# Kernel optimization log

Measured on AMD Instinct MI355X. Metric: run time of the kernel, lower is better.

The kernel has to match this reference:

```python
import jax, jax.numpy as jnp
from jax import lax
import numpy as np

IOU_THRESHOLD = 0.35
SCORE_THRESHOLD = 0.5


def _pairwise_iou(b):
    # b: [N,4] boxes in (ymin, xmin, ymax, xmax) convention (tf boxes)
    y1, x1, y2, x2 = b[:, 0], b[:, 1], b[:, 2], b[:, 3]
    area = (y2 - y1) * (x2 - x1)
    iy1 = jnp.maximum(y1[:, None], y1[None, :])
    ix1 = jnp.maximum(x1[:, None], x1[None, :])
    iy2 = jnp.minimum(y2[:, None], y2[None, :])
    ix2 = jnp.minimum(x2[:, None], x2[None, :])
    inter = jnp.maximum(iy2 - iy1, 0.0) * jnp.maximum(ix2 - ix1, 0.0)
    union = area[:, None] + area[None, :] - inter
    return jnp.where(union > 0, inter / union, 0.0)  # [N,N]


def _nms_sample_image(scores, boxes, anchors_wh, num_samples):
    # scores [N], boxes [N,4], anchors_wh [N,2]
    N = scores.shape[0]
    order = jnp.argsort(-scores)  # descending by score, like tf NMS
    s = scores[order]
    b = boxes[order]
    a = anchors_wh[order]
    valid = s > SCORE_THRESHOLD
    iou = _pairwise_iou(b)  # [N,N] on score-sorted boxes
    idx = jnp.arange(N)

    # greedy suppression: box i kept iff valid and no earlier kept box overlaps > thr
    def step(keep, i):
        suppressed = jnp.any(keep & (idx < i) & (iou[i] > IOU_THRESHOLD))
        return keep.at[i].set(valid[i] & ~suppressed), None

    keep, _ = lax.scan(step, jnp.zeros(N, dtype=bool), idx)

    # gather kept entries in (descending-score) order, then pad/slice to num_samples
    rank = jnp.cumsum(keep) - 1  # output slot for each kept entry
    slot = jnp.where(keep, jnp.minimum(rank, num_samples), num_samples)
    vals = jnp.concatenate([s[:, None], b, a], axis=1)  # [N,7]
    out = jnp.zeros((num_samples + 1, 7), vals.dtype).at[slot].set(vals)
    return out[:num_samples]  # [num_samples, 7] = (score | box(4) | anchor_wh(2))


def reference(scores, boxes, anchors, num_samples):
    # scores [B,H,W,1], boxes [B,H,W,4], anchors [B,H,W,4] (last 2 chans = w,h)
    B = scores.shape[0]
    sc = scores.reshape(B, -1)
    bx = boxes.reshape(B, -1, 4)
    an = anchors[..., 2:].reshape(B, -1, 2)
    out = jax.vmap(lambda s, b, a: _nms_sample_image(s, b, a, num_samples))(sc, bx, an)
    return out  # [B, num_samples, 7]


def setup_inputs() -> dict:
    key = jax.random.key(0)
    k1, k2, k3, k4, k5 = jax.random.split(key, 5)
    B, H, W = 8, 64, 64
    scores = jax.random.uniform(k1, (B, H, W, 1), dtype=jnp.float32)
    # well-formed tf boxes: ymin<ymax, xmin<xmax in [0,1]
    ymin = jax.random.uniform(k2, (B, H, W, 1), dtype=jnp.float32) * 0.8
    xmin = jax.random.uniform(k3, (B, H, W, 1), dtype=jnp.float32) * 0.8
    hh = jax.random.uniform(k4, (B, H, W, 1), dtype=jnp.float32) * 0.18 + 0.02
    ww = jax.random.uniform(k5, (B, H, W, 1), dtype=jnp.float32) * 0.18 + 0.02
    boxes = jnp.concatenate([ymin, xmin, ymin + hh, xmin + ww], axis=-1)
    # anchors: [cy, cx, w, h]-style; only last two channels are used
    k6 = jax.random.fold_in(key, 6)
    anchors = jax.random.uniform(k6, (B, H, W, 4), dtype=jnp.float32) * 0.25 + 0.05
    return {"scores": scores, "boxes": boxes, "anchors": anchors, "num_samples": 300}
```

## Files before the change

### kernel.cpp

```cpp
#include <hip/hip_runtime.h>

static constexpr float kIouT = 0.35f;
static constexpr float kScoreT = 0.5f;
static constexpr int kMaxNW = 48;
static constexpr int kStride = 49;
static constexpr int kMaxKeep = 512;

__device__ __forceinline__ float iou_f(const float4 a, const float4 b) {
  float areaA = __fmul_rn(a.z - a.x, a.w - a.y);
  float areaB = __fmul_rn(b.z - b.x, b.w - b.y);
  float iy1 = fmaxf(a.x, b.x);
  float ix1 = fmaxf(a.y, b.y);
  float iy2 = fminf(a.z, b.z);
  float ix2 = fminf(a.w, b.w);
  float dy = fmaxf(iy2 - iy1, 0.0f);
  float dx = fmaxf(ix2 - ix1, 0.0f);
  float inter = __fmul_rn(dy, dx);
  float uni = (areaA + areaB) - inter;
  return (uni > 0.0f) ? __fdiv_rn(inter, uni) : 0.0f;
}

__global__ __launch_bounds__(256)
void nms_count_kernel(const float* __restrict__ scores, int* __restrict__ Mcnt,
                      int N) {
  __shared__ int part[4];
  const int img = blockIdx.x, tid = threadIdx.x, lane = tid & 63, wv = tid >> 6;
  const float4* sc4 = (const float4*)(scores + (size_t)img * N);
  int c = 0;
  for (int q = tid; q < (N >> 2); q += 256) {
    float4 v = sc4[q];
    c += (v.x > kScoreT) + (v.y > kScoreT) + (v.z > kScoreT) + (v.w > kScoreT);
  }
#pragma unroll
  for (int off = 1; off < 64; off <<= 1) c += __shfl_xor(c, off, 64);
  if (lane == 0) part[wv] = c;
  __syncthreads();
  if (tid == 0) Mcnt[img] = part[0] + part[1] + part[2] + part[3];
}

__global__ __launch_bounds__(256)
void nms_rank_kernel(const float* __restrict__ scores,
                     const float4* __restrict__ boxes,
                     unsigned long long* __restrict__ skeys,
                     float4* __restrict__ sboxes, int N) {
  const int wid = (int)(((unsigned)blockIdx.x * blockDim.x + threadIdx.x) >> 6);
  const int lane = threadIdx.x & 63;
  const int img = wid / N;
  const int row = wid - img * N;
  const float* sc = scores + (size_t)img * N;
  const float si = sc[row];
  if (!(si > kScoreT)) return;
  const float4* sc4 = (const float4*)sc;
  int cnt = 0;
  for (int q = lane; q < (N >> 2); q += 64) {
    const float4 v = sc4[q];
    const int j = q << 2;
    cnt += (v.x > si) + (v.y > si) + (v.z > si) + (v.w > si);
    if (v.x == si && j < row) cnt++;
    if (v.y == si && j + 1 < row) cnt++;
    if (v.z == si && j + 2 < row) cnt++;
    if (v.w == si && j + 3 < row) cnt++;
  }
#pragma unroll
  for (int off = 1; off < 64; off <<= 1) cnt += __shfl_xor(cnt, off, 64);
  if (lane == 0) {
    skeys[(size_t)img * N + cnt] =
        ((unsigned long long)(~__float_as_uint(si)) << 32) | (unsigned)row;
    sboxes[(size_t)img * N + cnt] = boxes[(size_t)img * N + row];
  }
}

__global__ __launch_bounds__(256)
void nms_mask_kernel(const float4* __restrict__ sboxes,
                     const int* __restrict__ Mcnt,
                     unsigned long long* __restrict__ mask,
                     int N, int totalRows) {
  const int wid = (int)(((unsigned)blockIdx.x * blockDim.x + threadIdx.x) >> 6);
  const int lane = threadIdx.x & 63;
  if (wid >= totalRows) return;
  const int img = wid / N;
  const int row = wid - img * N;
  const int m = Mcnt[img];
  if (row >= m) return;
  const float4* sb = sboxes + (size_t)img * N;
  const float4 bi = sb[row];
  const int nw = (m + 63) >> 6;
  unsigned long long* mrow = mask + (size_t)wid * (size_t)(N >> 6);
  for (int w = row >> 6; w < nw; ++w) {
    int j = (w << 6) | lane;
    bool sup = false;
    if (j > row && j < m) sup = iou_f(bi, sb[j]) > kIouT;
    unsigned long long bm = __ballot(sup);
    if (lane == 0) mrow[w] = bm;
  }
}

__global__ __launch_bounds__(128)
void nms_scan_kernel(const unsigned long long* __restrict__ skeys,
                     const float4* __restrict__ sboxes,
                     const int* __restrict__ Mcnt,
                     const unsigned long long* __restrict__ mask,
                     const float* __restrict__ anchors,
                     float* __restrict__ out, int N, int NS) {
  __shared__ unsigned long long lbuf[2 * 64 * kStride];
  __shared__ int keptlist[kMaxKeep];
  __shared__ int s_done, s_kept;
  const int img = blockIdx.x;
  const int tid = threadIdx.x;
  const int lane = tid & 63;
  const int wv = tid >> 6;
  const int m = Mcnt[img];
  const int nw = (m + 63) >> 6;
  const int stride = N >> 6;
  const unsigned long long* mbase = mask + (size_t)img * (size_t)N * stride;
  const unsigned long long* kg = skeys + (size_t)img * N;
  const float4* sb = sboxes + (size_t)img * N;
  const float* an = anchors + (size_t)img * (size_t)N * 4;
  float* o = out + (size_t)img * NS * 7;
  if (tid == 0) { s_done = 0; s_kept = 0; }

  int kept = 0;
  unsigned long long remv = 0ull;

  if (m > 0 && nw <= kMaxNW) {
    const int nch = nw;
    if (wv == 1) {
      const int w = lane;
      if (w < nw) {
        const int rlim = (m < 64) ? m : 64;
        const unsigned long long* g = mbase + w;
        unsigned long long* dst = lbuf + w;
        for (int r = 0; r < rlim; ++r)
          dst[(size_t)r * kStride] = g[(size_t)r * stride];
      }
    }
    __syncthreads();
    for (int c = 0; c < nch; ++c) {
      if (wv == 0) {
        const unsigned long long* buf = lbuf + (size_t)(c & 1) * 64 * kStride;
        const unsigned long long diag = buf[(size_t)lane * kStride + c];
        unsigned long long local = __shfl(remv, c, 64);
        const int rem = m - (c << 6);
        const int lim = rem < 64 ? rem : 64;
        unsigned long long avail = ~local;
        if (lim < 64) avail &= ((1ull << lim) - 1ull);
        while (avail != 0ull && kept < NS) {
          const int b = __builtin_ctzll(avail);
          if (lane == 0) keptlist[kept] = (c << 6) + b;
          kept++;
          const unsigned long long rc = __shfl(diag, b, 64);
          if (lane > c && lane < nw)
            remv |= buf[(size_t)b * kStride + lane];
          local |= rc;
          avail &= ~local;
          avail &= ~(1ull << b);
        }
        if (lane == 0 && kept >= NS) s_done = 1;
      } else if (wv == 1 && c + 1 < nch) {
        const int cc = c + 1;
        const int w = cc + lane;
        if (w < nw) {
          const int base = cc << 6;
          int rlim = m - base;
          if (rlim > 64) rlim = 64;
          const unsigned long long* g = mbase + (size_t)base * stride + w;
          unsigned long long* dst = lbuf + (size_t)(cc & 1) * 64 * kStride + w;
          for (int r = 0; r < rlim; ++r)
            dst[(size_t)r * kStride] = g[(size_t)r * stride];
        }
      }
      __syncthreads();
      if (s_done) break;
    }
  } else if (m > 0) {
    if (wv == 0) {
      for (int i = 0; i < m && kept < NS; ++i) {
        const unsigned long long rw = __shfl(remv, i >> 6, 64);
        if ((rw >> (i & 63)) & 1ull) continue;
        if (lane == 0) keptlist[kept] = i;
        kept++;
        const unsigned long long* mrow = mbase + (size_t)i * stride;
        if (lane >= (i >> 6) && lane < nw) remv |= mrow[lane];
      }
    }
  }

  if (wv == 0 && lane == 0) s_kept = kept;
  __syncthreads();
  const int K = s_kept;
  for (int t = tid; t < K; t += 128) {
    const int i = keptlist[t];
    const unsigned long long ki = kg[i];
    const float4 bi = sb[i];
    const unsigned idx = (unsigned)ki;
    float* row = o + t * 7;
    row[0] = __uint_as_float(~(unsigned)(ki >> 32));
    row[1] = bi.x; row[2] = bi.y; row[3] = bi.z; row[4] = bi.w;
    row[5] = an[idx * 4 + 2];
    row[6] = an[idx * 4 + 3];
  }
  for (int t = K * 7 + tid; t < NS * 7; t += 128) o[t] = 0.0f;
}

__global__ __launch_bounds__(1024)
void nms_fused_kernel(const float* __restrict__ scores,
                      const float4* __restrict__ boxes,
                      const float* __restrict__ anchors,
                      float* __restrict__ out, int N, int NS) {
  __shared__ unsigned long long keys[4096];
  __shared__ int s_m;
  if (N > 4096) return;
  const int img = blockIdx.x;
  const int tid = threadIdx.x;
  const float* sc = scores + (size_t)img * N;
  const float4* bx = boxes + (size_t)img * N;
  if (tid == 0) s_m = 0;
  __syncthreads();
  int cnt = 0;
  for (int i = tid; i < N; i += blockDim.x) {
    float s = sc[i];
    keys[i] = ((unsigned long long)(~__float_as_uint(s)) << 32) | (unsigned)i;
    if (s > kScoreT) cnt++;
  }
  if (cnt) atomicAdd(&s_m, cnt);
  __syncthreads();
  for (int k = 2; k <= N; k <<= 1) {
    for (int j = k >> 1; j > 0; j >>= 1) {
      for (int i = tid; i < N; i += blockDim.x) {
        int ixj = i ^ j;
        if (ixj > i) {
          unsigned long long a = keys[i];
          unsigned long long b = keys[ixj];
          bool up = ((i & k) == 0);
          if (up ? (a > b) : (a < b)) { keys[i] = b; keys[ixj] = a; }
        }
      }
      __syncthreads();
    }
  }
  if (tid >= 64) return;
  const int lane = tid;
  const int m = s_m;
  const int nw = (m + 63) >> 6;
  const float* an = anchors + (size_t)img * N * 4;
  float* o = out + (size_t)img * NS * 7;
  unsigned long long remv = 0ull;
  int kept = 0;
  for (int i = 0; i < m && kept < NS; ++i) {
    unsigned long long rw = __shfl(remv, i >> 6, 64);
    if ((rw >> (i & 63)) & 1ull) continue;
    unsigned long long ki = keys[i];
    float4 bi = bx[(unsigned)ki];
    if (lane == 0) {
      unsigned idx = (unsigned)ki;
      float* row = o + kept * 7;
      row[0] = __uint_as_float(~(unsigned)(ki >> 32));
      row[1] = bi.x; row[2] = bi.y; row[3] = bi.z; row[4] = bi.w;
      row[5] = an[idx * 4 + 2];
      row[6] = an[idx * 4 + 3];
    }
    kept++;
    for (int w2 = i >> 6; w2 < nw; ++w2) {
      int j = (w2 << 6) | lane;
      bool sup = false;
      if (j > i && j < m) sup = iou_f(bi, bx[(unsigned)keys[j]]) > kIouT;
      unsigned long long bm = __ballot(sup);
      if (lane == w2) remv |= bm;
    }
  }
  for (int t = kept * 7 + lane; t < NS * 7; t += 64) o[t] = 0.0f;
}

extern "C" void kernel_launch(void* const* d_in, const int* in_sizes, int n_in,
                              void* d_out, int out_size, void* d_ws, size_t ws_size,
                              hipStream_t stream) {
  const float* scores = (const float*)d_in[0];
  const float4* boxes = (const float4*)d_in[1];
  const float* anchors = (const float*)d_in[2];
  float* out = (float*)d_out;
  const int B = 8;
  const int N = in_sizes[0] / B;
  const int NS = out_size / (B * 7);

  const size_t nTot = (size_t)B * (size_t)N;
  const size_t keysB = nTot * 8;
  const size_t sboxB = nTot * 16;
  const size_t mcntB = 256;
  const size_t maskB = nTot * (size_t)(N >> 6) * 8;
  const size_t need = keysB + sboxB + mcntB + maskB;

  if (ws_size >= need && (N % 256) == 0 && N >= 256 && NS <= kMaxKeep) {
    char* p = (char*)d_ws;
    unsigned long long* skeys = (unsigned long long*)p; p += keysB;
    float4* sboxes = (float4*)p;                         p += sboxB;
    int* Mcnt = (int*)p;                                 p += mcntB;
    unsigned long long* mask = (unsigned long long*)p;

    nms_count_kernel<<<B, 256, 0, stream>>>(scores, Mcnt, N);
    const int totalRows = B * N;
    const int rankBlocks = (int)(((long long)totalRows * 64 + 255) / 256);
    nms_rank_kernel<<<rankBlocks, 256, 0, stream>>>(scores, boxes, skeys,
                                                    sboxes, N);
    nms_mask_kernel<<<rankBlocks, 256, 0, stream>>>(sboxes, Mcnt, mask, N,
                                                    totalRows);
    nms_scan_kernel<<<B, 128, 0, stream>>>(skeys, sboxes, Mcnt, mask, anchors,
                                           out, N, NS);
  } else {
    nms_fused_kernel<<<B, 1024, 0, stream>>>(scores, boxes, anchors, out, N, NS);
  }
}
```

Before: 114.4 us.

## Use seven producer waves with register-staged triple-buffered mask prefetch in NMS scan

The scan kernel grows from 2 to 8 waves. Seven producer waves now load mask rows into registers two chunks ahead and commit them to a triple-buffered LDS ring, replacing the single wave that copied one row at a time. This spreads global loads across more waves and hides more latency behind the serial greedy wave. In exchange, the maximum supported word count drops from 48 to 36, so larger valid counts fall back to the slower global-memory path, and the block uses more registers.

```diff
diff --git a/kernel.cpp b/kernel.cpp
--- a/kernel.cpp
+++ b/kernel.cpp
@@ -2,8 +2,11 @@
 
 static constexpr float kIouT = 0.35f;
 static constexpr float kScoreT = 0.5f;
-static constexpr int kMaxNW = 48;
-static constexpr int kStride = 49;
+static constexpr int kMaxNW = 36;
+static constexpr int kStrideW = 37;
+static constexpr int kDepth = 3;
+static constexpr int kProdWaves = 7;
+static constexpr int kRowsPW = 10;
 static constexpr int kMaxKeep = 512;
 
 __device__ __forceinline__ float iou_f(const float4 a, const float4 b) {
@@ -95,14 +98,14 @@
   }
 }
 
-__global__ __launch_bounds__(128)
+__global__ __launch_bounds__(512)
 void nms_scan_kernel(const unsigned long long* __restrict__ skeys,
                      const float4* __restrict__ sboxes,
                      const int* __restrict__ Mcnt,
                      const unsigned long long* __restrict__ mask,
                      const float* __restrict__ anchors,
                      float* __restrict__ out, int N, int NS) {
-  __shared__ unsigned long long lbuf[2 * 64 * kStride];
+  __shared__ unsigned long long lbuf[kDepth * 64 * kStrideW];
   __shared__ int keptlist[kMaxKeep];
   __shared__ int s_done, s_kept;
   const int img = blockIdx.x;
@@ -123,51 +126,61 @@
   unsigned long long remv = 0ull;
 
   if (m > 0 && nw <= kMaxNW) {
-    const int nch = nw;
-    if (wv == 1) {
-      const int w = lane;
-      if (w < nw) {
-        const int rlim = (m < 64) ? m : 64;
-        const unsigned long long* g = mbase + w;
-        unsigned long long* dst = lbuf + w;
-        for (int r = 0; r < rlim; ++r)
-          dst[(size_t)r * kStride] = g[(size_t)r * stride];
-      }
+    const int pw = wv - 1;
+    unsigned long long pv[kRowsPW];
+    auto issue = [&](int cc) {
+      if (cc >= nw) return;
+      const int base = cc << 6;
+      const int rlim = min(m - base, 64);
+      const int w = cc + lane;
+      const bool wok = (w < nw);
+#pragma unroll
+      for (int k = 0; k < kRowsPW; ++k) {
+        const int r = pw + k * kProdWaves;
+        if (r < rlim && wok) pv[k] = mbase[(size_t)(base + r) * stride + w];
+      }
+    };
+    auto commit = [&](int cc) {
+      if (cc >= nw) return;
+      const int base = cc << 6;
+      const int rlim = min(m - base, 64);
+      const int w = cc + lane;
+      const bool wok = (w < nw);
+      unsigned long long* dst = lbuf + (size_t)(cc % kDepth) * 64 * kStrideW;
+#pragma unroll
+      for (int k = 0; k < kRowsPW; ++k) {
+        const int r = pw + k * kProdWaves;
+        if (r < rlim && wok) dst[(size_t)r * kStrideW + w] = pv[k];
+      }
+    };
+    if (wv != 0) {
+      issue(0); commit(0);
+      issue(1);
     }
     __syncthreads();
-    for (int c = 0; c < nch; ++c) {
+    for (int c = 0; c < nw; ++c) {
       if (wv == 0) {
-        const unsigned long long* buf = lbuf + (size_t)(c & 1) * 64 * kStride;
-        const unsigned long long diag = buf[(size_t)lane * kStride + c];
+        const unsigned long long* buf = lbuf + (size_t)(c % kDepth) * 64 * kStrideW;
+        const unsigned long long diag = buf[(size_t)lane * kStrideW + c];
         unsigned long long local = __shfl(remv, c, 64);
         const int rem = m - (c << 6);
-        const int lim = rem < 64 ? rem : 64;
         unsigned long long avail = ~local;
-        if (lim < 64) avail &= ((1ull << lim) - 1ull);
+        if (rem < 64) avail &= ((1ull << rem) - 1ull);
         while (avail != 0ull && kept < NS) {
           const int b = __builtin_ctzll(avail);
           if (lane == 0) keptlist[kept] = (c << 6) + b;
           kept++;
           const unsigned long long rc = __shfl(diag, b, 64);
           if (lane > c && lane < nw)
-            remv |= buf[(size_t)b * kStride + lane];
+            remv |= buf[(size_t)b * kStrideW + lane];
           local |= rc;
           avail &= ~local;
           avail &= ~(1ull << b);
         }
         if (lane == 0 && kept >= NS) s_done = 1;
-      } else if (wv == 1 && c + 1 < nch) {
-        const int cc = c + 1;
-        const int w = cc + lane;
-        if (w < nw) {
-          const int base = cc << 6;
-          int rlim = m - base;
-          if (rlim > 64) rlim = 64;
-          const unsigned long long* g = mbase + (size_t)base * stride + w;
-          unsigned long long* dst = lbuf + (size_t)(cc & 1) * 64 * kStride + w;
-          for (int r = 0; r < rlim; ++r)
-            dst[(size_t)r * kStride] = g[(size_t)r * stride];
-        }
+      } else {
+        commit(c + 1);
+        issue(c + 2);
       }
       __syncthreads();
       if (s_done) break;
@@ -188,7 +201,7 @@
   if (wv == 0 && lane == 0) s_kept = kept;
   __syncthreads();
   const int K = s_kept;
-  for (int t = tid; t < K; t += 128) {
+  for (int t = tid; t < K; t += 512) {
     const int i = keptlist[t];
     const unsigned long long ki = kg[i];
     const float4 bi = sb[i];
@@ -199,7 +212,7 @@
     row[5] = an[idx * 4 + 2];
     row[6] = an[idx * 4 + 3];
   }
-  for (int t = K * 7 + tid; t < NS * 7; t += 128) o[t] = 0.0f;
+  for (int t = K * 7 + tid; t < NS * 7; t += 512) o[t] = 0.0f;
 }
 
 __global__ __launch_bounds__(1024)
@@ -303,7 +316,7 @@
                                                     sboxes, N);
     nms_mask_kernel<<<rankBlocks, 256, 0, stream>>>(sboxes, Mcnt, mask, N,
                                                     totalRows);
-    nms_scan_kernel<<<B, 128, 0, stream>>>(skeys, sboxes, Mcnt, mask, anchors,
+    nms_scan_kernel<<<B, 512, 0, stream>>>(skeys, sboxes, Mcnt, mask, anchors,
                                            out, N, NS);
   } else {
     nms_fused_kernel<<<B, 1024, 0, stream>>>(scores, boxes, anchors, out, N, NS);
```

After: 114.1 us. Within noise of the previous version (-0.3%).

## Fold score count into rank kernel and make scan single-wave with register diagonals

Applied to the files above, without the earlier changes.

The separate count kernel is merged into the rank kernel as extra blocks, which removes one launch. The scan kernel drops from two waves with an LDS double buffer and per-chunk __syncthreads to a single wave. That wave keeps the diagonal mask words in registers, prefetched three chunks ahead, and reads them with readlane. Row mask words for kept boxes are then gathered from global memory in batches of eight to overlap latency. This removes the barriers and LDS staging, at the cost of serial global loads landing on the critical path of the greedy scan.

```diff
diff --git a/kernel.cpp b/kernel.cpp
--- a/kernel.cpp
+++ b/kernel.cpp
@@ -2,8 +2,6 @@
 
 static constexpr float kIouT = 0.35f;
 static constexpr float kScoreT = 0.5f;
-static constexpr int kMaxNW = 48;
-static constexpr int kStride = 49;
 static constexpr int kMaxKeep = 512;
 
 __device__ __forceinline__ float iou_f(const float4 a, const float4 b) {
@@ -20,31 +18,39 @@
   return (uni > 0.0f) ? __fdiv_rn(inter, uni) : 0.0f;
 }
 
-__global__ __launch_bounds__(256)
-void nms_count_kernel(const float* __restrict__ scores, int* __restrict__ Mcnt,
-                      int N) {
-  __shared__ int part[4];
-  const int img = blockIdx.x, tid = threadIdx.x, lane = tid & 63, wv = tid >> 6;
-  const float4* sc4 = (const float4*)(scores + (size_t)img * N);
-  int c = 0;
-  for (int q = tid; q < (N >> 2); q += 256) {
-    float4 v = sc4[q];
-    c += (v.x > kScoreT) + (v.y > kScoreT) + (v.z > kScoreT) + (v.w > kScoreT);
-  }
-#pragma unroll
-  for (int off = 1; off < 64; off <<= 1) c += __shfl_xor(c, off, 64);
-  if (lane == 0) part[wv] = c;
-  __syncthreads();
-  if (tid == 0) Mcnt[img] = part[0] + part[1] + part[2] + part[3];
+__device__ __forceinline__ unsigned long long rdlane64(unsigned long long v,
+                                                       int l) {
+  unsigned lo = (unsigned)__builtin_amdgcn_readlane((int)(unsigned)v, l);
+  unsigned hi = (unsigned)__builtin_amdgcn_readlane((int)(unsigned)(v >> 32), l);
+  return ((unsigned long long)hi << 32) | lo;
 }
 
 __global__ __launch_bounds__(256)
 void nms_rank_kernel(const float* __restrict__ scores,
                      const float4* __restrict__ boxes,
                      unsigned long long* __restrict__ skeys,
-                     float4* __restrict__ sboxes, int N) {
-  const int wid = (int)(((unsigned)blockIdx.x * blockDim.x + threadIdx.x) >> 6);
-  const int lane = threadIdx.x & 63;
+                     float4* __restrict__ sboxes,
+                     int* __restrict__ Mcnt, int N, int rankBlocks) {
+  const int tid = threadIdx.x;
+  const int lane = tid & 63;
+  if ((int)blockIdx.x >= rankBlocks) {
+    __shared__ int part[4];
+    const int img = blockIdx.x - rankBlocks;
+    const int wv = tid >> 6;
+    const float4* sc4 = (const float4*)(scores + (size_t)img * N);
+    int c = 0;
+    for (int q = tid; q < (N >> 2); q += 256) {
+      float4 v = sc4[q];
+      c += (v.x > kScoreT) + (v.y > kScoreT) + (v.z > kScoreT) + (v.w > kScoreT);
+    }
+#pragma unroll
+    for (int off = 1; off < 64; off <<= 1) c += __shfl_xor(c, off, 64);
+    if (lane == 0) part[wv] = c;
+    __syncthreads();
+    if (tid == 0) Mcnt[img] = part[0] + part[1] + part[2] + part[3];
+    return;
+  }
+  const int wid = (int)(((unsigned)blockIdx.x * blockDim.x + tid) >> 6);
   const int img = wid / N;
   const int row = wid - img * N;
   const float* sc = scores + (size_t)img * N;
@@ -95,21 +101,18 @@
   }
 }
 
-__global__ __launch_bounds__(128)
+__global__ __launch_bounds__(64)
 void nms_scan_kernel(const unsigned long long* __restrict__ skeys,
                      const float4* __restrict__ sboxes,
                      const int* __restrict__ Mcnt,
                      const unsigned long long* __restrict__ mask,
                      const float* __restrict__ anchors,
                      float* __restrict__ out, int N, int NS) {
-  __shared__ unsigned long long lbuf[2 * 64 * kStride];
   __shared__ int keptlist[kMaxKeep];
-  __shared__ int s_done, s_kept;
   const int img = blockIdx.x;
-  const int tid = threadIdx.x;
-  const int lane = tid & 63;
-  const int wv = tid >> 6;
-  const int m = Mcnt[img];
+  const int lane = threadIdx.x;
+  int m = Mcnt[img];
+  if (m > N) m = N;
   const int nw = (m + 63) >> 6;
   const int stride = N >> 6;
   const unsigned long long* mbase = mask + (size_t)img * (size_t)N * stride;
@@ -117,78 +120,63 @@
   const float4* sb = sboxes + (size_t)img * N;
   const float* an = anchors + (size_t)img * (size_t)N * 4;
   float* o = out + (size_t)img * NS * 7;
-  if (tid == 0) { s_done = 0; s_kept = 0; }
 
   int kept = 0;
   unsigned long long remv = 0ull;
 
-  if (m > 0 && nw <= kMaxNW) {
-    const int nch = nw;
-    if (wv == 1) {
-      const int w = lane;
-      if (w < nw) {
-        const int rlim = (m < 64) ? m : 64;
-        const unsigned long long* g = mbase + w;
-        unsigned long long* dst = lbuf + w;
-        for (int r = 0; r < rlim; ++r)
-          dst[(size_t)r * kStride] = g[(size_t)r * stride];
+  if (m > 0) {
+    auto dgload = [&](int cc) -> unsigned long long {
+      return (cc < nw) ? mbase[(size_t)((cc << 6) + lane) * stride + cc] : 0ull;
+    };
+    unsigned long long dg0 = dgload(0);
+    unsigned long long dg1 = dgload(1);
+    unsigned long long dg2 = dgload(2);
+
+    for (int c = 0; c < nw && kept < NS; ++c) {
+      const int cb = c << 6;
+      unsigned long long local = rdlane64(remv, c);
+      const int rem = m - cb;
+      unsigned long long avail = ~local;
+      if (rem < 64) avail &= (1ull << rem) - 1ull;
+      unsigned long long keptbits = 0ull;
+      while (avail != 0ull && kept < NS) {
+        const int b = (int)__builtin_ctzll(avail);
+        if (lane == 0) keptlist[kept] = cb + b;
+        kept++;
+        keptbits |= 1ull << b;
+        const unsigned long long rc = rdlane64(dg0, b);
+        local |= rc;
+        avail &= ~local;
+        avail &= ~(1ull << b);
       }
-    }
-    __syncthreads();
-    for (int c = 0; c < nch; ++c) {
-      if (wv == 0) {
-        const unsigned long long* buf = lbuf + (size_t)(c & 1) * 64 * kStride;
-        const unsigned long long diag = buf[(size_t)lane * kStride + c];
-        unsigned long long local = __shfl(remv, c, 64);
-        const int rem = m - (c << 6);
-        const int lim = rem < 64 ? rem : 64;
-        unsigned long long avail = ~local;
-        if (lim < 64) avail &= ((1ull << lim) - 1ull);
-        while (avail != 0ull && kept < NS) {
-          const int b = __builtin_ctzll(avail);
-          if (lane == 0) keptlist[kept] = (c << 6) + b;
-          kept++;
-          const unsigned long long rc = __shfl(diag, b, 64);
-          if (lane > c && lane < nw)
-            remv |= buf[(size_t)b * kStride + lane];
-          local |= rc;
-          avail &= ~local;
-          avail &= ~(1ull << b);
+      dg0 = dg1; dg1 = dg2; dg2 = dgload(c + 3);
+      const bool lok = (lane > c) && (lane < nw);
+      while (keptbits != 0ull) {
+        unsigned long long t[8];
+        int bs[8];
+#pragma unroll
+        for (int k = 0; k < 8; ++k) {
+          if (keptbits != 0ull) {
+            bs[k] = (int)__builtin_ctzll(keptbits);
+            keptbits &= keptbits - 1ull;
+          } else {
+            bs[k] = -1;
+          }
         }
-        if (lane == 0 && kept >= NS) s_done = 1;
-      } else if (wv == 1 && c + 1 < nch) {
-        const int cc = c + 1;
-        const int w = cc + lane;
-        if (w < nw) {
-          const int base = cc << 6;
-          int rlim = m - base;
-          if (rlim > 64) rlim = 64;
-          const unsigned long long* g = mbase + (size_t)base * stride + w;
-          unsigned long long* dst = lbuf + (size_t)(cc & 1) * 64 * kStride + w;
-          for (int r = 0; r < rlim; ++r)
-            dst[(size_t)r * kStride] = g[(size_t)r * stride];
-        }
+#pragma unroll
+        for (int k = 0; k < 8; ++k)
+          t[k] = (bs[k] >= 0 && lok)
+                     ? mbase[(size_t)(cb + bs[k]) * stride + lane]
+                     : 0ull;
+#pragma unroll
+        for (int k = 0; k < 8; ++k)
+          if (bs[k] >= 0) remv |= t[k];
       }
-      __syncthreads();
-      if (s_done) break;
-    }
-  } else if (m > 0) {
-    if (wv == 0) {
-      for (int i = 0; i < m && kept < NS; ++i) {
-        const unsigned long long rw = __shfl(remv, i >> 6, 64);
-        if ((rw >> (i & 63)) & 1ull) continue;
-        if (lane == 0) keptlist[kept] = i;
-        kept++;
-        const unsigned long long* mrow = mbase + (size_t)i * stride;
-        if (lane >= (i >> 6) && lane < nw) remv |= mrow[lane];
-      }
-    }
-  }
-
-  if (wv == 0 && lane == 0) s_kept = kept;
+    }
+  }
+
   __syncthreads();
-  const int K = s_kept;
-  for (int t = tid; t < K; t += 128) {
+  for (int t = lane; t < kept; t += 64) {
     const int i = keptlist[t];
     const unsigned long long ki = kg[i];
     const float4 bi = sb[i];
@@ -199,7 +187,7 @@
     row[5] = an[idx * 4 + 2];
     row[6] = an[idx * 4 + 3];
   }
-  for (int t = K * 7 + tid; t < NS * 7; t += 128) o[t] = 0.0f;
+  for (int t = kept * 7 + lane; t < NS * 7; t += 64) o[t] = 0.0f;
 }
 
 __global__ __launch_bounds__(1024)
@@ -289,22 +277,23 @@
   const size_t maskB = nTot * (size_t)(N >> 6) * 8;
   const size_t need = keysB + sboxB + mcntB + maskB;
 
-  if (ws_size >= need && (N % 256) == 0 && N >= 256 && NS <= kMaxKeep) {
+  if (ws_size >= need && (N % 256) == 0 && N >= 256 && N <= 4096 &&
+      NS <= kMaxKeep) {
     char* p = (char*)d_ws;
     unsigned long long* skeys = (unsigned long long*)p; p += keysB;
     float4* sboxes = (float4*)p;                         p += sboxB;
     int* Mcnt = (int*)p;                                 p += mcntB;
     unsigned long long* mask = (unsigned long long*)p;
 
-    nms_count_kernel<<<B, 256, 0, stream>>>(scores, Mcnt, N);
     const int totalRows = B * N;
-    const int rankBlocks = (int)(((long long)totalRows * 64 + 255) / 256);
-    nms_rank_kernel<<<rankBlocks, 256, 0, stream>>>(scores, boxes, skeys,
-                                                    sboxes, N);
+    const int rankBlocks = totalRows / 4;
+    nms_rank_kernel<<<rankBlocks + B, 256, 0, stream>>>(scores, boxes, skeys,
+                                                        sboxes, Mcnt, N,
+                                                        rankBlocks);
     nms_mask_kernel<<<rankBlocks, 256, 0, stream>>>(sboxes, Mcnt, mask, N,
                                                     totalRows);
-    nms_scan_kernel<<<B, 128, 0, stream>>>(skeys, sboxes, Mcnt, mask, anchors,
-                                           out, N, NS);
+    nms_scan_kernel<<<B, 64, 0, stream>>>(skeys, sboxes, Mcnt, mask, anchors,
+                                          out, N, NS);
   } else {
     nms_fused_kernel<<<B, 1024, 0, stream>>>(scores, boxes, anchors, out, N, NS);
   }
```

Measured after the change: 108.2 us. -5.4%, faster.
